# Kernel tuning notes

Hardware: AMD Instinct MI355X
Metric: run time of the kernel (lower is better)

The kernel has to match this reference:

```python
import jax, jax.numpy as jnp
import numpy as np

N_EMBED = 2048
NUM_EXPERTS = 64
TOP_K = 8
B, S = 4, 4096


def setup_inputs() -> dict:
    key = jax.random.key(0)
    k_x, k_n, k_w1, k_b1, k_w2, k_b2 = jax.random.split(key, 6)
    bound = 1.0 / np.sqrt(N_EMBED)  # torch nn.Linear default init range
    return {
        "x": jax.random.normal(k_x, (B, S, N_EMBED), dtype=jnp.float32),
        "noise": jax.random.normal(k_n, (B, S, NUM_EXPERTS), dtype=jnp.float32),
        "W1": jax.random.uniform(k_w1, (N_EMBED, NUM_EXPERTS), jnp.float32, -bound, bound),
        "b1": jax.random.uniform(k_b1, (NUM_EXPERTS,), jnp.float32, -bound, bound),
        "W2": jax.random.uniform(k_w2, (N_EMBED, NUM_EXPERTS), jnp.float32, -bound, bound),
        "b2": jax.random.uniform(k_b2, (NUM_EXPERTS,), jnp.float32, -bound, bound),
    }


def reference(x, noise, W1, b1, W2, b2):
    # logits = lin1(x); noise_scale = softplus(lin2(x))
    logits = jnp.einsum("bsd,de->bse", x, W1) + b1          # [B,S,E]
    scale = jax.nn.softplus(jnp.einsum("bsd,de->bse", x, W2) + b2)
    mixed = logits + noise * scale                            # [B,S,E]
    full = jax.nn.softmax(mixed, axis=-1)

    topk_vals, topk_idx = jax.lax.top_k(mixed, TOP_K)         # [B,S,K]

    # scatter topk values into a -inf background, then softmax (masked softmax)
    E = mixed.shape[-1]
    flat_mixed = mixed.reshape(-1, E)
    flat_idx = topk_idx.reshape(-1, TOP_K)
    flat_vals = topk_vals.reshape(-1, TOP_K)
    rows = jnp.arange(flat_mixed.shape[0])[:, None]
    sparse = jnp.full_like(flat_mixed, -jnp.inf).at[rows, flat_idx].set(flat_vals)
    sparse_sm = jax.nn.softmax(sparse, axis=-1).reshape(mixed.shape)

    return sparse_sm, topk_idx, full
```

## Files before the change

### kernel.cpp

```cpp
#include <hip/hip_runtime.h>
#include <math.h>


typedef _Float16 f16x8 __attribute__((ext_vector_type(8)));
typedef _Float16 f16x4 __attribute__((ext_vector_type(4)));
typedef float f32x4 __attribute__((ext_vector_type(4)));

constexpr int ND = 2048, NE = 64, NK = 8, NTOK = 16384;
constexpr int KC   = 32;
constexpr int NCHT = ND / KC;
constexpr int KS   = 2;
constexpr int CPS  = NCHT / KS;
constexpr int MTOK = 32;
constexpr int XROW = 40;
constexpr int XPLANE = MTOK * XROW;
constexpr int XBUF   = 2 * XPLANE;

__global__ void prep_w(const float* __restrict__ W1, const float* __restrict__ W2,
                       _Float16* __restrict__ wt3) {
    const int g    = blockIdx.x * 256 + threadIdx.x;
    const int cg   = g >> 9;
    const int rem  = g & 511;
    const int t    = rem >> 6;
    const int lane = rem & 63;
    const int col  = lane & 15, q = lane >> 4;
    const int n    = t * 16 + col;
    const float* W = (t < 4) ? W1 : W2;
    const int cn   = n & 63;
    _Float16 h[8], l[8];
    #pragma unroll
    for (int j = 0; j < 8; ++j) {
        const float v = W[(size_t)(cg * 32 + q * 8 + j) * 64 + cn];
        const _Float16 hh = (_Float16)v;
        h[j] = hh;
        l[j] = (_Float16)((v - (float)hh) * 2048.0f);
    }
    *(f16x8*)&wt3[((size_t)(cg * 2 + 0) * 8 + t) * 512 + lane * 8] = *(f16x8*)h;
    *(f16x8*)&wt3[((size_t)(cg * 2 + 1) * 8 + t) * 512 + lane * 8] = *(f16x8*)l;
}

__global__ __launch_bounds__(256, 4)
void router_main(const float* __restrict__ x, const _Float16* __restrict__ wt3,
                 float* __restrict__ zpart) {
    __shared__ _Float16 xlds[2 * XBUF];
    const int tid  = threadIdx.x;
    const int lane = tid & 63;
    const int wu   = __builtin_amdgcn_readfirstlane(tid >> 6);
    const int col  = lane & 15, q = lane >> 4;
    const int mg   = blockIdx.x >> 1;
    const int ks   = blockIdx.x & 1;
    const long tok0 = (long)mg * MTOK;
    const int c0   = ks * CPS;
    const int ta   = 2 * wu, tb = 2 * wu + 1;

    const int ltok = tid >> 3;
    const int lsub = tid & 7;
    const float* xbase = x + (tok0 + ltok) * (size_t)ND + (size_t)c0 * KC + lsub * 4;

    f32x4 a0[2][2], a1[2][2];
    #pragma unroll
    for (int m = 0; m < 2; ++m)
        #pragma unroll
        for (int i = 0; i < 2; ++i)
            #pragma unroll
            for (int r = 0; r < 4; ++r) { a0[m][i][r] = 0.f; a1[m][i][r] = 0.f; }

    float4 xv = *(const float4*)xbase;

    for (int c = 0; c < CPS; ++c) {
        _Float16* xb = &xlds[(c & 1) * XBUF];

        {
            const _Float16 h0 = (_Float16)xv.x, h1 = (_Float16)xv.y,
                           h2 = (_Float16)xv.z, h3 = (_Float16)xv.w;
            const f16x4 hv = {h0, h1, h2, h3};
            const f16x4 lv = { (_Float16)((xv.x - (float)h0) * 2048.0f),
                               (_Float16)((xv.y - (float)h1) * 2048.0f),
                               (_Float16)((xv.z - (float)h2) * 2048.0f),
                               (_Float16)((xv.w - (float)h3) * 2048.0f) };
            *(f16x4*)&xb[ltok * XROW + lsub * 4]          = hv;
            *(f16x4*)&xb[XPLANE + ltok * XROW + lsub * 4] = lv;
        }
        __syncthreads();

        const size_t fb = (size_t)(c0 + c) * 2 * 8 * 512 + (size_t)lane * 8;
        const f16x8 bha = *(const f16x8*)&wt3[fb + ta * 512];
        const f16x8 bhb = *(const f16x8*)&wt3[fb + tb * 512];
        const f16x8 bla = *(const f16x8*)&wt3[fb + 8 * 512 + ta * 512];
        const f16x8 blb = *(const f16x8*)&wt3[fb + 8 * 512 + tb * 512];

        if (c + 1 < CPS) xv = *(const float4*)(xbase + (c + 1) * KC);

        #pragma unroll
        for (int mt = 0; mt < 2; ++mt) {
            const f16x8 ah = *(const f16x8*)&xb[(mt * 16 + col) * XROW + q * 8];
            const f16x8 al = *(const f16x8*)&xb[XPLANE + (mt * 16 + col) * XROW + q * 8];
            a0[mt][0] = __builtin_amdgcn_mfma_f32_16x16x32_f16(ah, bha, a0[mt][0], 0, 0, 0);
            a0[mt][1] = __builtin_amdgcn_mfma_f32_16x16x32_f16(ah, bhb, a0[mt][1], 0, 0, 0);
            a1[mt][0] = __builtin_amdgcn_mfma_f32_16x16x32_f16(ah, bla, a1[mt][0], 0, 0, 0);
            a1[mt][1] = __builtin_amdgcn_mfma_f32_16x16x32_f16(ah, blb, a1[mt][1], 0, 0, 0);
            a1[mt][0] = __builtin_amdgcn_mfma_f32_16x16x32_f16(al, bha, a1[mt][0], 0, 0, 0);
            a1[mt][1] = __builtin_amdgcn_mfma_f32_16x16x32_f16(al, bhb, a1[mt][1], 0, 0, 0);
        }
        __syncthreads();
    }

    float* zp = zpart + (size_t)ks * NTOK * 128;
    #pragma unroll
    for (int mt = 0; mt < 2; ++mt)
        #pragma unroll
        for (int i = 0; i < 2; ++i) {
            const int n = (2 * wu + i) * 16 + col;
            #pragma unroll
            for (int r = 0; r < 4; ++r) {
                const long token = tok0 + mt * 16 + q * 4 + r;
                zp[(size_t)token * 128 + n] = a0[mt][i][r] + a1[mt][i][r] * 4.8828125e-4f;
            }
        }
}

__global__ __launch_bounds__(256, 4)
void router_epi(const float* __restrict__ zpart, const float* __restrict__ noise,
                const float* __restrict__ b1, const float* __restrict__ b2,
                float* __restrict__ out_sparse, float* __restrict__ out_idx,
                float* __restrict__ out_full) {
    const int lane = threadIdx.x & 63;
    const int wu   = threadIdx.x >> 6;
    const float b1v = b1[lane];
    const float b2v = b2[lane];

    for (int tt = 0; tt < 4; ++tt) {
        const long tok = (long)blockIdx.x * 16 + wu * 4 + tt;
        const size_t r0 = (size_t)tok * 128;
        const size_t s1 = (size_t)NTOK * 128;
        const double z1d = (double)zpart[r0 + lane]      + (double)zpart[s1 + r0 + lane];
        const double z2d = (double)zpart[r0 + 64 + lane] + (double)zpart[s1 + r0 + 64 + lane];
        const float z1 = (float)z1d + b1v;
        const float z2 = (float)z2d + b2v;
        const float sc = (float)log1p(exp((double)z2));
        const float nz = noise[tok * NE + lane];
        const float mixed = z1 + nz * sc;

        float vmax = mixed;
        for (int off = 32; off; off >>= 1) vmax = fmaxf(vmax, __shfl_xor(vmax, off));
        const float e = expf(mixed - vmax);
        float denom = e;
        for (int off = 32; off; off >>= 1) denom += __shfl_xor(denom, off);
        const float fullv = e / denom;

        float cur = mixed;
        int   sel = 0;
        float myidxf = 0.0f;
        #pragma unroll
        for (int r = 0; r < NK; ++r) {
            float bv = cur; int bi = lane;
            for (int off = 32; off; off >>= 1) {
                const float ov = __shfl_xor(bv, off);
                const int   oi = __shfl_xor(bi, off);
                if (ov > bv || (ov == bv && oi < bi)) { bv = ov; bi = oi; }
            }
            if (lane == r)  myidxf = (float)bi;
            if (lane == bi) { sel = 1; cur = -INFINITY; }
        }

        const float es = sel ? e : 0.0f;
        float dsum = es;
        for (int off = 32; off; off >>= 1) dsum += __shfl_xor(dsum, off);
        const float sparsev = sel ? (e / dsum) : 0.0f;

        out_full[tok * NE + lane]   = fullv;
        out_sparse[tok * NE + lane] = sparsev;
        if (lane < NK) out_idx[tok * NK + lane] = myidxf;
    }
}

extern "C" void kernel_launch(void* const* d_in, const int* in_sizes, int n_in,
                              void* d_out, int out_size, void* d_ws, size_t ws_size,
                              hipStream_t stream) {
    const float* x     = (const float*)d_in[0];
    const float* noise = (const float*)d_in[1];
    const float* W1    = (const float*)d_in[2];
    const float* b1    = (const float*)d_in[3];
    const float* W2    = (const float*)d_in[4];
    const float* b2    = (const float*)d_in[5];

    float* out_sparse = (float*)d_out;
    float* out_idx    = out_sparse + (size_t)NTOK * NE;
    float* out_full   = out_idx + (size_t)NTOK * NK;

    _Float16* wt3 = (_Float16*)d_ws;
    float* zpart  = (float*)((char*)d_ws + ((size_t)1 << 20));

    prep_w<<<128, 256, 0, stream>>>(W1, W2, wt3);
    router_main<<<NTOK / MTOK * KS, 256, 0, stream>>>(x, wt3, zpart);
    router_epi<<<NTOK / 16, 256, 0, stream>>>(zpart, noise, b1, b2,
                                              out_sparse, out_idx, out_full);
}
```

Before: 255.8 us.

## Load x directly into MFMA registers, drop LDS staging, halve token tile

The router GEMM kernel now has each lane load its own 8 x values straight from global memory in the MFMA A-operand layout and split them into hi/lo fp16 in registers. This removes the LDS double buffer and both __syncthreads per chunk. The token tile is halved to 16 so each wave does one M-tile, launch bounds ask for 5 blocks/SM, and partial sums are flushed into double accumulators every 8 chunks for accuracy. The cost is strided, less coalesced global loads (each lane reads 32 bytes from a different row), twice as many blocks, and weight loads reused over half as many tokens.

```diff
diff --git a/kernel.cpp b/kernel.cpp
--- a/kernel.cpp
+++ b/kernel.cpp
@@ -3,7 +3,6 @@
 
 
 typedef _Float16 f16x8 __attribute__((ext_vector_type(8)));
-typedef _Float16 f16x4 __attribute__((ext_vector_type(4)));
 typedef float f32x4 __attribute__((ext_vector_type(4)));
 
 constexpr int ND = 2048, NE = 64, NK = 8, NTOK = 16384;
@@ -11,10 +10,7 @@
 constexpr int NCHT = ND / KC;
 constexpr int KS   = 2;
 constexpr int CPS  = NCHT / KS;
-constexpr int MTOK = 32;
-constexpr int XROW = 40;
-constexpr int XPLANE = MTOK * XROW;
-constexpr int XBUF   = 2 * XPLANE;
+constexpr int MTOK = 16;
 
 __global__ void prep_w(const float* __restrict__ W1, const float* __restrict__ W2,
                        _Float16* __restrict__ wt3) {
@@ -39,10 +35,9 @@
     *(f16x8*)&wt3[((size_t)(cg * 2 + 1) * 8 + t) * 512 + lane * 8] = *(f16x8*)l;
 }
 
-__global__ __launch_bounds__(256, 4)
+__global__ __launch_bounds__(256, 5)
 void router_main(const float* __restrict__ x, const _Float16* __restrict__ wt3,
                  float* __restrict__ zpart) {
-    __shared__ _Float16 xlds[2 * XBUF];
     const int tid  = threadIdx.x;
     const int lane = tid & 63;
     const int wu   = __builtin_amdgcn_readfirstlane(tid >> 6);
@@ -51,72 +46,73 @@
     const int ks   = blockIdx.x & 1;
     const long tok0 = (long)mg * MTOK;
     const int c0   = ks * CPS;
-    const int ta   = 2 * wu, tb = 2 * wu + 1;
+    const int ta   = 2 * wu;
 
-    const int ltok = tid >> 3;
-    const int lsub = tid & 7;
-    const float* xbase = x + (tok0 + ltok) * (size_t)ND + (size_t)c0 * KC + lsub * 4;
+    const float* xrow = x + (tok0 + col) * (size_t)ND + (size_t)c0 * KC + q * 8;
 
-    f32x4 a0[2][2], a1[2][2];
+    f32x4 a0[2], a1[2];
+    double zm[2][4];
     #pragma unroll
-    for (int m = 0; m < 2; ++m)
+    for (int i = 0; i < 2; ++i)
         #pragma unroll
-        for (int i = 0; i < 2; ++i)
-            #pragma unroll
-            for (int r = 0; r < 4; ++r) { a0[m][i][r] = 0.f; a1[m][i][r] = 0.f; }
+        for (int r = 0; r < 4; ++r) { a0[i][r] = 0.f; a1[i][r] = 0.f; zm[i][r] = 0.0; }
 
-    float4 xv = *(const float4*)xbase;
+    float4 xa = *(const float4*)(xrow);
+    float4 xb = *(const float4*)(xrow + 4);
 
     for (int c = 0; c < CPS; ++c) {
-        _Float16* xb = &xlds[(c & 1) * XBUF];
+        const size_t fb = (size_t)(c0 + c) * 8192 + (size_t)lane * 8;
+        const f16x8 bha = *(const f16x8*)&wt3[fb + ta * 512];
+        const f16x8 bhb = *(const f16x8*)&wt3[fb + (ta + 1) * 512];
+        const f16x8 bla = *(const f16x8*)&wt3[fb + 4096 + ta * 512];
+        const f16x8 blb = *(const f16x8*)&wt3[fb + 4096 + (ta + 1) * 512];
 
-        {
-            const _Float16 h0 = (_Float16)xv.x, h1 = (_Float16)xv.y,
-                           h2 = (_Float16)xv.z, h3 = (_Float16)xv.w;
-            const f16x4 hv = {h0, h1, h2, h3};
-            const f16x4 lv = { (_Float16)((xv.x - (float)h0) * 2048.0f),
-                               (_Float16)((xv.y - (float)h1) * 2048.0f),
-                               (_Float16)((xv.z - (float)h2) * 2048.0f),
-                               (_Float16)((xv.w - (float)h3) * 2048.0f) };
-            *(f16x4*)&xb[ltok * XROW + lsub * 4]          = hv;
-            *(f16x4*)&xb[XPLANE + ltok * XROW + lsub * 4] = lv;
+        float4 na, nb;
+        if (c + 1 < CPS) {
+            na = *(const float4*)(xrow + (c + 1) * KC);
+            nb = *(const float4*)(xrow + (c + 1) * KC + 4);
         }
-        __syncthreads();
 
-        const size_t fb = (size_t)(c0 + c) * 2 * 8 * 512 + (size_t)lane * 8;
-        const f16x8 bha = *(const f16x8*)&wt3[fb + ta * 512];
-        const f16x8 bhb = *(const f16x8*)&wt3[fb + tb * 512];
-        const f16x8 bla = *(const f16x8*)&wt3[fb + 8 * 512 + ta * 512];
-        const f16x8 blb = *(const f16x8*)&wt3[fb + 8 * 512 + tb * 512];
+        const float xf[8] = {xa.x, xa.y, xa.z, xa.w, xb.x, xb.y, xb.z, xb.w};
+        f16x8 ah, al;
+        #pragma unroll
+        for (int j = 0; j < 8; ++j) {
+            const _Float16 h = (_Float16)xf[j];
+            ah[j] = h;
+            al[j] = (_Float16)((xf[j] - (float)h) * 2048.0f);
+        }
 
-        if (c + 1 < CPS) xv = *(const float4*)(xbase + (c + 1) * KC);
+        a0[0] = __builtin_amdgcn_mfma_f32_16x16x32_f16(ah, bha, a0[0], 0, 0, 0);
+        a0[1] = __builtin_amdgcn_mfma_f32_16x16x32_f16(ah, bhb, a0[1], 0, 0, 0);
+        a1[0] = __builtin_amdgcn_mfma_f32_16x16x32_f16(ah, bla, a1[0], 0, 0, 0);
+        a1[1] = __builtin_amdgcn_mfma_f32_16x16x32_f16(ah, blb, a1[1], 0, 0, 0);
+        a1[0] = __builtin_amdgcn_mfma_f32_16x16x32_f16(al, bha, a1[0], 0, 0, 0);
+        a1[1] = __builtin_amdgcn_mfma_f32_16x16x32_f16(al, bhb, a1[1], 0, 0, 0);
 
-        #pragma unroll
-        for (int mt = 0; mt < 2; ++mt) {
-            const f16x8 ah = *(const f16x8*)&xb[(mt * 16 + col) * XROW + q * 8];
-            const f16x8 al = *(const f16x8*)&xb[XPLANE + (mt * 16 + col) * XROW + q * 8];
-            a0[mt][0] = __builtin_amdgcn_mfma_f32_16x16x32_f16(ah, bha, a0[mt][0], 0, 0, 0);
-            a0[mt][1] = __builtin_amdgcn_mfma_f32_16x16x32_f16(ah, bhb, a0[mt][1], 0, 0, 0);
-            a1[mt][0] = __builtin_amdgcn_mfma_f32_16x16x32_f16(ah, bla, a1[mt][0], 0, 0, 0);
-            a1[mt][1] = __builtin_amdgcn_mfma_f32_16x16x32_f16(ah, blb, a1[mt][1], 0, 0, 0);
-            a1[mt][0] = __builtin_amdgcn_mfma_f32_16x16x32_f16(al, bha, a1[mt][0], 0, 0, 0);
-            a1[mt][1] = __builtin_amdgcn_mfma_f32_16x16x32_f16(al, bhb, a1[mt][1], 0, 0, 0);
+        xa = na; xb = nb;
+
+        if ((c & 7) == 7) {
+            #pragma unroll
+            for (int i = 0; i < 2; ++i)
+                #pragma unroll
+                for (int r = 0; r < 4; ++r) {
+                    zm[i][r] += (double)a0[i][r]
+                              + (double)(a1[i][r] * 4.8828125e-4f);
+                    a0[i][r] = 0.f; a1[i][r] = 0.f;
+                }
         }
-        __syncthreads();
     }
 
     float* zp = zpart + (size_t)ks * NTOK * 128;
     #pragma unroll
-    for (int mt = 0; mt < 2; ++mt)
+    for (int i = 0; i < 2; ++i) {
+        const int n = (ta + i) * 16 + col;
         #pragma unroll
-        for (int i = 0; i < 2; ++i) {
-            const int n = (2 * wu + i) * 16 + col;
-            #pragma unroll
-            for (int r = 0; r < 4; ++r) {
-                const long token = tok0 + mt * 16 + q * 4 + r;
-                zp[(size_t)token * 128 + n] = a0[mt][i][r] + a1[mt][i][r] * 4.8828125e-4f;
-            }
+        for (int r = 0; r < 4; ++r) {
+            const long token = tok0 + q * 4 + r;
+            zp[(size_t)token * 128 + n] = (float)zm[i][r];
         }
+    }
 }
 
 __global__ __launch_bounds__(256, 4)
```

After: 312.8 us. +22.3%, slower.
